# Performance work log

Measured on AMD Instinct MI355X. Metric: run time of the kernel, lower is better.

The kernel has to match this reference:

```python
import jax, jax.numpy as jnp
import numpy as np

D_MODEL = 128
N_HEADS = 8
HEAD_DIM = D_MODEL // N_HEADS
N_EXPERTS = 256
B, T = 4, 512


def rmsnorm(x, gamma, eps=1e-6):
    norm = jnp.sqrt(jnp.mean(jnp.square(x), axis=-1, keepdims=True) + eps)
    return gamma * (x / norm)


def apply_rope(x):
    # x: (B, T, H, D) -- half-split (NeoX-style) rotation
    Bx, Tx, Hx, Dx = x.shape
    inv_freq = 1.0 / (10000.0 ** (jnp.arange(0, Dx, 2, dtype=jnp.float32) / Dx))
    t = jnp.arange(Tx, dtype=jnp.float32)
    freqs = jnp.outer(t, inv_freq)                      # (T, D/2)
    sin_f = jnp.sin(freqs)[None, :, None, :]            # (1, T, 1, D/2)
    cos_f = jnp.cos(freqs)[None, :, None, :]
    x1, x2 = jnp.split(x, 2, axis=-1)
    return jnp.concatenate([x1 * cos_f - x2 * sin_f, x1 * sin_f + x2 * cos_f], axis=-1)


def swiglu(x, w1, b1, w2, b2):
    gate = x @ w1 + b1
    return gate * jax.nn.sigmoid(gate) * (x @ w2 + b2)


def lightning_attention(x, wq, bq, wk, bk, wv, bv, wo, bo):
    Bx, Tx, _ = x.shape
    q = (x @ wq + bq).reshape(Bx, Tx, N_HEADS, HEAD_DIM)
    k = (x @ wk + bk).reshape(Bx, Tx, N_HEADS, HEAD_DIM)
    v = (x @ wv + bv).reshape(Bx, Tx, N_HEADS, HEAD_DIM)
    q = jax.nn.elu(apply_rope(q)) + 1.0
    k = jax.nn.elu(apply_rope(k)) + 1.0
    q = q.transpose(0, 2, 1, 3)  # (B,H,T,D)
    k = k.transpose(0, 2, 1, 3)
    v = v.transpose(0, 2, 1, 3)
    ctx = jnp.einsum('bhtd,bhte->bhde', k, v)           # (B,H,D,D)
    out = jnp.einsum('bhtd,bhde->bhte', q, ctx)         # (B,H,T,D)
    k_sum = jnp.sum(k, axis=2)                          # (B,H,D)
    z = 1.0 / (jnp.einsum('bhtd,bhd->bht', q, k_sum) + 1e-6)
    out = out * z[..., None]
    out = out.transpose(0, 2, 1, 3).reshape(Bx, Tx, D_MODEL)
    return out @ wo + bo


def turbo_quant(x, rot, scale):
    y = x @ rot
    mag = jnp.sqrt(jnp.mean(jnp.square(y), axis=-1, keepdims=True) + 1e-6)
    phase = y / mag
    quant = jnp.round(phase * 8.0) / 8.0
    phase = jax.lax.stop_gradient(quant - phase) + phase  # STE
    return phase * mag * scale


def gated_moe(h, gate_w, gate_b, exp_w, mw1, mb1, mw2, mb2):
    gate_scores = jax.nn.softmax(h @ gate_w + gate_b, axis=-1)       # (B,T,E)
    top_vals, top_idx = jax.lax.top_k(gate_scores, 2)                # (B,T,2)
    top_w = top_vals / (jnp.sum(top_vals, axis=-1, keepdims=True) + 1e-6)
    onehot = jax.nn.one_hot(top_idx, N_EXPERTS, dtype=h.dtype)       # (B,T,2,E)
    mask = jnp.sum(onehot * top_w[..., None], axis=2)                # (B,T,E)
    expert_outputs = jnp.einsum('btd,edo->bteo', h, exp_w)           # (B,T,E,D)
    weighted_avg = jnp.einsum('bteo,bte->bto', expert_outputs, mask)
    weighted_avg = swiglu(weighted_avg, mw1, mb1, mw2, mb2)
    diff_sq = jnp.square(expert_outputs - weighted_avg[:, :, None, :])
    weighted_var = jnp.einsum('bteo,bte->bto', diff_sq, mask)
    consensus = jnp.exp(-jnp.mean(weighted_var, axis=-1))            # (B,T)
    return weighted_avg, consensus


def setup_inputs() -> dict:
    key = jax.random.key(0)
    ks = jax.random.split(key, 24)
    d = D_MODEL
    dw = lambda k, shp: (jax.random.normal(k, shp, dtype=jnp.float32) * 0.02)
    rng = np.random.RandomState(42)
    Q, _ = np.linalg.qr(rng.randn(d, d))
    return {
        'x': jax.random.normal(ks[0], (B, T, d), dtype=jnp.float32),
        'g1': jnp.ones((d,), jnp.float32),
        'wq': dw(ks[1], (d, d)), 'bq': jnp.zeros((d,), jnp.float32),
        'wk': dw(ks[2], (d, d)), 'bk': jnp.zeros((d,), jnp.float32),
        'wv': dw(ks[3], (d, d)), 'bv': jnp.zeros((d,), jnp.float32),
        'wo': dw(ks[4], (d, d)), 'bo': jnp.zeros((d,), jnp.float32),
        'rot': jnp.asarray(Q.astype('float32')),
        'tq_scale': jnp.ones((d,), jnp.float32),
        'sw_w1': dw(ks[5], (d, d)), 'sw_b1': jnp.zeros((d,), jnp.float32),
        'sw_w2': dw(ks[6], (d, d)), 'sw_b2': jnp.zeros((d,), jnp.float32),
        'g2': jnp.ones((d,), jnp.float32),
        'gate_w': dw(ks[7], (d, N_EXPERTS)), 'gate_b': jnp.zeros((N_EXPERTS,), jnp.float32),
        'exp_w': dw(ks[8], (N_EXPERTS, d, d)),
        'moe_w1': dw(ks[9], (d, d)), 'moe_b1': jnp.zeros((d,), jnp.float32),
        'moe_w2': dw(ks[10], (d, d)), 'moe_b2': jnp.zeros((d,), jnp.float32),
    }


def reference(x, g1, wq, bq, wk, bk, wv, bv, wo, bo, rot, tq_scale,
              sw_w1, sw_b1, sw_w2, sw_b2, g2, gate_w, gate_b, exp_w,
              moe_w1, moe_b1, moe_w2, moe_b2):
    attn_out = lightning_attention(rmsnorm(x, g1), wq, bq, wk, bk, wv, bv, wo, bo)
    attn_out = turbo_quant(attn_out, rot, tq_scale)
    x = x + swiglu(attn_out, sw_w1, sw_b1, sw_w2, sw_b2)
    moe_out, consensus = gated_moe(rmsnorm(x, g2), gate_w, gate_b, exp_w,
                                   moe_w1, moe_b1, moe_w2, moe_b2)
    x = x + moe_out
    return x, consensus
```

## Files before the change

kernel.cpp:

```cpp
#include <hip/hip_runtime.h>
#include <math.h>

#define DM 128
#define SEQ 512
#define NTOK 2048
#define NH 8
#define HD 16
#define NE 256
#define CAP 4096

__device__ __forceinline__ float sigmoid_f(float v) { return 1.0f / (1.0f + expf(-v)); }

__device__ __forceinline__ float wave_sum64(float v) {
#pragma unroll
  for (int m = 32; m; m >>= 1) v += __shfl_xor(v, m, 64);
  return v;
}

__global__ __launch_bounds__(512) void k_qkv(
    const float* __restrict__ x, const float* __restrict__ g1,
    const float* __restrict__ wq, const float* __restrict__ bq,
    const float* __restrict__ wk, const float* __restrict__ bk,
    const float* __restrict__ wv, const float* __restrict__ bv_,
    float* __restrict__ q, float* __restrict__ k, float* __restrict__ v) {
  const int tid = threadIdx.x;
  const int o = tid & 127, ks = tid >> 7;
  const int n0 = blockIdx.x * 4;
  __shared__ float h1[4][DM];
  __shared__ float qr[4][DM], kr[4][DM];
  __shared__ float red3[4][4][DM][3];
  __shared__ float wredA[8];

  float xv = x[(n0 + ks) * DM + o];
  float s = wave_sum64(xv * xv);
  if ((tid & 63) == 0) wredA[tid >> 6] = s;
  __syncthreads();
  float tot = wredA[2 * ks] + wredA[2 * ks + 1];
  float rinv = 1.0f / sqrtf(tot * (1.0f / 128.0f) + 1e-6f);
  h1[ks][o] = g1[o] * xv * rinv;
  __syncthreads();

  float aq[4] = {0, 0, 0, 0}, ak[4] = {0, 0, 0, 0}, av[4] = {0, 0, 0, 0};
  const int d0 = ks * 32;
  for (int dd = 0; dd < 32; ++dd) {
    int d = d0 + dd;
    float wqv = wq[d * DM + o], wkv = wk[d * DM + o], wvv = wv[d * DM + o];
#pragma unroll
    for (int g = 0; g < 4; ++g) {
      float hv = h1[g][d];
      aq[g] = fmaf(hv, wqv, aq[g]);
      ak[g] = fmaf(hv, wkv, ak[g]);
      av[g] = fmaf(hv, wvv, av[g]);
    }
  }
#pragma unroll
  for (int g = 0; g < 4; ++g) {
    red3[ks][g][o][0] = aq[g];
    red3[ks][g][o][1] = ak[g];
    red3[ks][g][o][2] = av[g];
  }
  __syncthreads();
  float sq = bq[o], sk = bk[o], sv = bv_[o];
#pragma unroll
  for (int s2 = 0; s2 < 4; ++s2) {
    sq += red3[s2][ks][o][0];
    sk += red3[s2][ks][o][1];
    sv += red3[s2][ks][o][2];
  }
  qr[ks][o] = sq;
  kr[ks][o] = sk;
  v[(n0 + ks) * DM + o] = sv;
  __syncthreads();

  const int i = o & 15, j = i & 7, hi = i & 8, lo = o & ~8;
  const float invf = expf(-(float)j * 1.1512925464970229f);
  int t = (n0 + ks) & (SEQ - 1);
  float ang = (float)t * invf;
  float sn = sinf(ang), cs = cosf(ang);
  float x1q = qr[ks][lo], x2q = qr[ks][lo + 8];
  float x1k = kr[ks][lo], x2k = kr[ks][lo + 8];
  float rq = hi ? (x1q * sn + x2q * cs) : (x1q * cs - x2q * sn);
  float rk = hi ? (x1k * sn + x2k * cs) : (x1k * cs - x2k * sn);
  rq = (rq > 0.0f) ? rq + 1.0f : expf(rq);
  rk = (rk > 0.0f) ? rk + 1.0f : expf(rk);
  q[(n0 + ks) * DM + o] = rq;
  k[(n0 + ks) * DM + o] = rk;
}

__global__ __launch_bounds__(256) void k_ctxp(
    const float* __restrict__ k, const float* __restrict__ v,
    float* __restrict__ ctxp, float* __restrict__ ksump) {
  const int bh = blockIdx.x & 31, tc = blockIdx.x >> 5;
  const int b = bh >> 3, h = bh & 7;
  const int p = threadIdx.x, d = p >> 4, e = p & 15;
  const float* kb = k + (size_t)b * SEQ * DM + h * HD;
  const float* vb = v + (size_t)b * SEQ * DM + h * HD;
  float acc = 0.0f, kss = 0.0f;
  for (int tt = 0; tt < 64; ++tt) {
    int t = tc * 64 + tt;
    float kv = kb[t * DM + d];
    float vv = vb[t * DM + e];
    acc = fmaf(kv, vv, acc);
    kss += kv;
  }
  ctxp[tc * 8192 + bh * 256 + p] = acc;
  if (e == 0) ksump[tc * 512 + bh * HD + d] = kss;
}

__global__ __launch_bounds__(512) void k_attn(
    const float* __restrict__ x, const float* __restrict__ qp,
    const float* __restrict__ ctxp, const float* __restrict__ ksump,
    const float* __restrict__ wo, const float* __restrict__ bo,
    const float* __restrict__ rot, const float* __restrict__ tqs,
    const float* __restrict__ w1, const float* __restrict__ b1,
    const float* __restrict__ w2, const float* __restrict__ b2,
    const float* __restrict__ g2,
    float* __restrict__ xmid, float* __restrict__ h2o) {
  const int tid = threadIdx.x;
  const int o = tid & 127, ks = tid >> 7;
  const int n0 = blockIdx.x * 4;
  const int b = n0 >> 9;
  __shared__ float ctxs[NH * 256];
  __shared__ float kss[DM];
  __shared__ float rowA[4][DM], rowB[4][DM];
  __shared__ float red2[4][4][DM][2];
  __shared__ float wredA[8], wredB[8];

  for (int idx = tid; idx < 2048; idx += 512) {
    float s = 0.0f;
#pragma unroll
    for (int tc = 0; tc < 8; ++tc) s += ctxp[tc * 8192 + b * 2048 + idx];
    ctxs[idx] = s;
  }
  if (tid < 128) {
    float s = 0.0f;
#pragma unroll
    for (int tc = 0; tc < 8; ++tc) s += ksump[tc * 512 + b * DM + tid];
    kss[tid] = s;
  }
  rowA[ks][o] = qp[(n0 + ks) * DM + o];
  __syncthreads();

  {
    int h = o >> 4, e = o & 15;
    float oa = 0.0f, qk = 0.0f;
#pragma unroll
    for (int d = 0; d < HD; ++d) {
      float qv = rowA[ks][h * HD + d];
      oa = fmaf(qv, ctxs[h * 256 + d * 16 + e], oa);
      qk = fmaf(qv, kss[h * HD + d], qk);
    }
    rowB[ks][o] = oa / (qk + 1e-6f);
  }
  __syncthreads();

  const int d0 = ks * 32;
  {
    float acc[4] = {0, 0, 0, 0};
    for (int dd = 0; dd < 32; ++dd) {
      int d = d0 + dd;
      float w = wo[d * DM + o];
#pragma unroll
      for (int g = 0; g < 4; ++g) acc[g] = fmaf(rowB[g][d], w, acc[g]);
    }
#pragma unroll
    for (int g = 0; g < 4; ++g) red2[ks][g][o][0] = acc[g];
  }
  __syncthreads();
  {
    float sa = bo[o];
#pragma unroll
    for (int s2 = 0; s2 < 4; ++s2) sa += red2[s2][ks][o][0];
    rowA[ks][o] = sa;
  }
  __syncthreads();

  {
    float acc[4] = {0, 0, 0, 0};
    for (int dd = 0; dd < 32; ++dd) {
      int d = d0 + dd;
      float r = rot[d * DM + o];
#pragma unroll
      for (int g = 0; g < 4; ++g) acc[g] = fmaf(rowA[g][d], r, acc[g]);
    }
#pragma unroll
    for (int g = 0; g < 4; ++g) red2[ks][g][o][1] = acc[g];
  }
  __syncthreads();
  {
    float y = 0.0f;
#pragma unroll
    for (int s2 = 0; s2 < 4; ++s2) y += red2[s2][ks][o][1];
    float ssq = wave_sum64(y * y);
    if ((tid & 63) == 0) wredA[tid >> 6] = ssq;
    __syncthreads();
    float tot = wredA[2 * ks] + wredA[2 * ks + 1];
    float mag = sqrtf(tot * (1.0f / 128.0f) + 1e-6f);
    float phase = y / mag;
    rowB[ks][o] = rintf(phase * 8.0f) * 0.125f * mag * tqs[o];
  }
  __syncthreads();

  {
    float a1[4] = {0, 0, 0, 0}, a2[4] = {0, 0, 0, 0};
    for (int dd = 0; dd < 32; ++dd) {
      int d = d0 + dd;
      float w1v = w1[d * DM + o];
      float w2v = w2[d * DM + o];
#pragma unroll
      for (int g = 0; g < 4; ++g) {
        float t = rowB[g][d];
        a1[g] = fmaf(t, w1v, a1[g]);
        a2[g] = fmaf(t, w2v, a2[g]);
      }
    }
#pragma unroll
    for (int g = 0; g < 4; ++g) {
      red2[ks][g][o][0] = a1[g];
      red2[ks][g][o][1] = a2[g];
    }
  }
  __syncthreads();
  {
    float ga = b1[o], up = b2[o];
#pragma unroll
    for (int s2 = 0; s2 < 4; ++s2) {
      ga += red2[s2][ks][o][0];
      up += red2[s2][ks][o][1];
    }
    float swv = ga * sigmoid_f(ga) * up;
    float xm = x[(n0 + ks) * DM + o] + swv;
    xmid[(n0 + ks) * DM + o] = xm;
    float ssq = wave_sum64(xm * xm);
    if ((tid & 63) == 0) wredB[tid >> 6] = ssq;
    __syncthreads();
    float tot = wredB[2 * ks] + wredB[2 * ks + 1];
    float rinv = 1.0f / sqrtf(tot * (1.0f / 128.0f) + 1e-6f);
    h2o[(n0 + ks) * DM + o] = g2[o] * xm * rinv;
  }
}

__global__ __launch_bounds__(1024) void k_gate(
    const float* __restrict__ h2, const float* __restrict__ gate_w,
    const float* __restrict__ gate_b,
    float* __restrict__ tw, int* __restrict__ cnt, int* __restrict__ list) {
  const int tid = threadIdx.x;
  const int n0 = blockIdx.x * 4;
  __shared__ float h2s[4][DM];
  __shared__ float redg[4][4][NE];
  __shared__ float lgl[4][NE];

  if (tid < 512) {
    int g = tid >> 7, o = tid & 127;
    h2s[g][o] = h2[(n0 + g) * DM + o];
  }
  __syncthreads();

  {
    int e = tid & 255, kq = tid >> 8;
    float lg[4] = {0, 0, 0, 0};
    for (int dd = 0; dd < 32; ++dd) {
      int d = kq * 32 + dd;
      float gw = gate_w[d * NE + e];
#pragma unroll
      for (int g = 0; g < 4; ++g) lg[g] = fmaf(h2s[g][d], gw, lg[g]);
    }
#pragma unroll
    for (int g = 0; g < 4; ++g) redg[kq][g][e] = lg[g];
  }
  __syncthreads();
  {
    int e = tid & 255, kq = tid >> 8;
    float lf = gate_b[e];
#pragma unroll
    for (int s2 = 0; s2 < 4; ++s2) lf += redg[s2][kq][e];
    lgl[kq][e] = lf;
  }
  __syncthreads();

  if (tid < 256) {
    int lane = tid & 63, g = tid >> 6;
    float bv = -INFINITY;
    int bi = 0;
#pragma unroll
    for (int j2 = 0; j2 < 4; ++j2) {
      int e = lane + 64 * j2;
      float vv = lgl[g][e];
      if (vv > bv || (vv == bv && e < bi)) { bv = vv; bi = e; }
    }
#pragma unroll
    for (int m = 32; m; m >>= 1) {
      float pv = __shfl_xor(bv, m, 64);
      int pi = __shfl_xor(bi, m, 64);
      if (pv > bv || (pv == bv && pi < bi)) { bv = pv; bi = pi; }
    }
    float se = 0.0f;
#pragma unroll
    for (int j2 = 0; j2 < 4; ++j2) se += expf(lgl[g][lane + 64 * j2] - bv);
    se = wave_sum64(se);
    float mv = -INFINITY;
    int mi = 0;
#pragma unroll
    for (int j2 = 0; j2 < 4; ++j2) {
      int e = lane + 64 * j2;
      if (e != bi) {
        float vv = lgl[g][e];
        if (vv > mv || (vv == mv && e < mi)) { mv = vv; mi = e; }
      }
    }
#pragma unroll
    for (int m = 32; m; m >>= 1) {
      float pv = __shfl_xor(mv, m, 64);
      int pi = __shfl_xor(mi, m, 64);
      if (pv > mv || (pv == mv && pi < mi)) { mv = pv; mi = pi; }
    }
    if (lane == 0) {
      float v0 = 1.0f / se;
      float v1 = expf(mv - bv) / se;
      float wsum = v0 + v1 + 1e-6f;
      int t = n0 + g;
      tw[t * 2 + 0] = v0 / wsum;
      tw[t * 2 + 1] = v1 / wsum;
      int r0 = atomicAdd(&cnt[bi], 1);
      list[bi * CAP + r0] = t * 2 + 0;
      int r1 = atomicAdd(&cnt[mi], 1);
      list[mi * CAP + r1] = t * 2 + 1;
    }
  }
}

__global__ __launch_bounds__(512) void k_exp(
    const float* __restrict__ h2, const float* __restrict__ exp_w,
    const int* __restrict__ cnt, const int* __restrict__ list,
    float* __restrict__ elbuf) {
  const int e = blockIdx.x;
  const int nt = cnt[e];
  if (nt == 0) return;
  const int tid = threadIdx.x;
  const int o = tid & 127, qq = tid >> 7;
  const float* W = exp_w + (size_t)e * (DM * DM);
  float wreg[32];
#pragma unroll
  for (int dd = 0; dd < 32; ++dd) wreg[dd] = W[(qq * 32 + dd) * DM + o];
  __shared__ float h2t[8][DM];
  __shared__ float psum[4][8][DM];
  __shared__ int alst[8];

  for (int i0 = 0; i0 < nt; i0 += 8) {
    int gn = min(8, nt - i0);
    for (int idx = tid; idx < gn * 128; idx += 512) {
      int j = idx >> 7;
      int a = list[e * CAP + i0 + j];
      h2t[j][idx & 127] = h2[(size_t)(a >> 1) * DM + (idx & 127)];
    }
    if (tid < gn) alst[tid] = list[e * CAP + i0 + tid];
    __syncthreads();
    for (int j = 0; j < gn; ++j) {
      const float4* hp = (const float4*)&h2t[j][qq * 32];
      float acc = 0.0f;
#pragma unroll
      for (int d4 = 0; d4 < 8; ++d4) {
        float4 hv = hp[d4];
        acc = fmaf(wreg[d4 * 4 + 0], hv.x, acc);
        acc = fmaf(wreg[d4 * 4 + 1], hv.y, acc);
        acc = fmaf(wreg[d4 * 4 + 2], hv.z, acc);
        acc = fmaf(wreg[d4 * 4 + 3], hv.w, acc);
      }
      psum[qq][j][o] = acc;
    }
    __syncthreads();
    for (int j = qq; j < gn; j += 4) {
      float r = psum[0][j][o] + psum[1][j][o] + psum[2][j][o] + psum[3][j][o];
      elbuf[(size_t)alst[j] * DM + o] = r;
    }
    __syncthreads();
  }
}

__global__ __launch_bounds__(512) void k_comb(
    const float* __restrict__ elbuf, const float* __restrict__ tw,
    const float* __restrict__ xmid,
    const float* __restrict__ mw1, const float* __restrict__ mb1,
    const float* __restrict__ mw2, const float* __restrict__ mb2,
    float* __restrict__ out_x, float* __restrict__ out_cons) {
  const int tid = threadIdx.x;
  const int g = tid >> 7, o = tid & 127;
  const int t = blockIdx.x * 4 + g;
  __shared__ float was[4][DM];
  __shared__ float wredV[8];
  float w0 = tw[t * 2 + 0], w1 = tw[t * 2 + 1];
  float el0 = elbuf[(size_t)(t * 2 + 0) * DM + o];
  float el1 = elbuf[(size_t)(t * 2 + 1) * DM + o];
  was[g][o] = w0 * el0 + w1 * el1;
  __syncthreads();
  float a1 = mb1[o], a2 = mb2[o];
  for (int d = 0; d < DM; ++d) {
    float tt = was[g][d];
    a1 = fmaf(tt, mw1[d * DM + o], a1);
    a2 = fmaf(tt, mw2[d * DM + o], a2);
  }
  float swv = a1 * sigmoid_f(a1) * a2;
  out_x[(size_t)t * DM + o] = xmid[(size_t)t * DM + o] + swv;
  float dd0 = el0 - swv, dd1 = el1 - swv;
  float vt = wave_sum64(w0 * dd0 * dd0 + w1 * dd1 * dd1);
  if ((tid & 63) == 0) wredV[tid >> 6] = vt;
  __syncthreads();
  if (tid < 4)
    out_cons[blockIdx.x * 4 + tid] =
        expf(-(wredV[2 * tid] + wredV[2 * tid + 1]) * (1.0f / 128.0f));
}

extern "C" void kernel_launch(void* const* d_in, const int* in_sizes, int n_in,
                              void* d_out, int out_size, void* d_ws, size_t ws_size,
                              hipStream_t stream) {
  const float* x = (const float*)d_in[0];
  const float* g1 = (const float*)d_in[1];
  const float* wq = (const float*)d_in[2];
  const float* bq = (const float*)d_in[3];
  const float* wk = (const float*)d_in[4];
  const float* bk = (const float*)d_in[5];
  const float* wv = (const float*)d_in[6];
  const float* bv = (const float*)d_in[7];
  const float* wo = (const float*)d_in[8];
  const float* bo = (const float*)d_in[9];
  const float* rot = (const float*)d_in[10];
  const float* tqs = (const float*)d_in[11];
  const float* sw1 = (const float*)d_in[12];
  const float* sb1 = (const float*)d_in[13];
  const float* sw2 = (const float*)d_in[14];
  const float* sb2 = (const float*)d_in[15];
  const float* g2 = (const float*)d_in[16];
  const float* gw = (const float*)d_in[17];
  const float* gb = (const float*)d_in[18];
  const float* ew = (const float*)d_in[19];
  const float* mw1 = (const float*)d_in[20];
  const float* mb1 = (const float*)d_in[21];
  const float* mw2 = (const float*)d_in[22];
  const float* mb2 = (const float*)d_in[23];

  float* ws = (float*)d_ws;
  float* q = ws;
  float* k = ws + 262144;
  float* v = ws + 524288;
  float* ctxp = ws + 786432;
  float* ksump = ws + 851968;
  float* xmid = ws + 856064;
  float* h2 = ws + 1118208;
  float* tw = ws + 1380352;
  float* elbuf = ws + 1384448;
  int* cnt = (int*)(ws + 1908736);
  int* list = (int*)(ws + 1908992);
  float* out_x = (float*)d_out;
  float* out_c = out_x + (size_t)NTOK * DM;

  hipMemsetAsync(cnt, 0, NE * sizeof(int), stream);
  hipLaunchKernelGGL(k_qkv, dim3(NTOK / 4), dim3(512), 0, stream,
                     x, g1, wq, bq, wk, bk, wv, bv, q, k, v);
  hipLaunchKernelGGL(k_ctxp, dim3(256), dim3(256), 0, stream, k, v, ctxp, ksump);
  hipLaunchKernelGGL(k_attn, dim3(NTOK / 4), dim3(512), 0, stream,
                     x, q, ctxp, ksump, wo, bo, rot, tqs, sw1, sb1, sw2, sb2, g2,
                     xmid, h2);
  hipLaunchKernelGGL(k_gate, dim3(NTOK / 4), dim3(1024), 0, stream,
                     h2, gw, gb, tw, cnt, list);
  hipLaunchKernelGGL(k_exp, dim3(NE), dim3(512), 0, stream,
                     h2, ew, cnt, list, elbuf);
  hipLaunchKernelGGL(k_comb, dim3(NTOK / 4), dim3(512), 0, stream,
                     elbuf, tw, xmid, mw1, mb1, mw2, mb2, out_x, out_c);
}
```

Measured before the change: 75.34 us.

## Fuse gating into attention kernel, drop memset, split-K the combine kernel

Moves the MoE gate logits, top-2 selection and expert list building into the tail of the attention kernel, reusing the h2 rows already in shared memory. This removes one kernel launch and the global reload of h2. The cnt buffer is now zeroed inside the first kernel instead of by a separate memset. The combine kernel grows to 1024 threads with a two-way split-K over the SwiGLU matmul. In exchange, the attention kernel uses more shared memory and does more work per block, which may lower occupancy.

Result: faster. 68.57 us (-9.0%).

```diff
diff --git a/kernel.cpp b/kernel.cpp
--- a/kernel.cpp
+++ b/kernel.cpp
@@ -22,7 +22,8 @@
     const float* __restrict__ wq, const float* __restrict__ bq,
     const float* __restrict__ wk, const float* __restrict__ bk,
     const float* __restrict__ wv, const float* __restrict__ bv_,
-    float* __restrict__ q, float* __restrict__ k, float* __restrict__ v) {
+    float* __restrict__ q, float* __restrict__ k, float* __restrict__ v,
+    int* __restrict__ cnt) {
   const int tid = threadIdx.x;
   const int o = tid & 127, ks = tid >> 7;
   const int n0 = blockIdx.x * 4;
@@ -30,6 +31,8 @@
   __shared__ float qr[4][DM], kr[4][DM];
   __shared__ float red3[4][4][DM][3];
   __shared__ float wredA[8];
+
+  if (blockIdx.x == 0 && tid < NE) cnt[tid] = 0;
 
   float xv = x[(n0 + ks) * DM + o];
   float s = wave_sum64(xv * xv);
@@ -115,7 +118,9 @@
     const float* __restrict__ w1, const float* __restrict__ b1,
     const float* __restrict__ w2, const float* __restrict__ b2,
     const float* __restrict__ g2,
-    float* __restrict__ xmid, float* __restrict__ h2o) {
+    const float* __restrict__ gate_w, const float* __restrict__ gate_b,
+    float* __restrict__ xmid, float* __restrict__ h2o,
+    float* __restrict__ tw, int* __restrict__ cnt, int* __restrict__ list) {
   const int tid = threadIdx.x;
   const int o = tid & 127, ks = tid >> 7;
   const int n0 = blockIdx.x * 4;
@@ -124,6 +129,8 @@
   __shared__ float kss[DM];
   __shared__ float rowA[4][DM], rowB[4][DM];
   __shared__ float red2[4][4][DM][2];
+  __shared__ float redg[2][4][NE];
+  __shared__ float lgl[4][NE];
   __shared__ float wredA[8], wredB[8];
 
   for (int idx = tid; idx < 2048; idx += 512) {
@@ -236,45 +243,33 @@
     __syncthreads();
     float tot = wredB[2 * ks] + wredB[2 * ks + 1];
     float rinv = 1.0f / sqrtf(tot * (1.0f / 128.0f) + 1e-6f);
-    h2o[(n0 + ks) * DM + o] = g2[o] * xm * rinv;
-  }
-}
-
-__global__ __launch_bounds__(1024) void k_gate(
-    const float* __restrict__ h2, const float* __restrict__ gate_w,
-    const float* __restrict__ gate_b,
-    float* __restrict__ tw, int* __restrict__ cnt, int* __restrict__ list) {
-  const int tid = threadIdx.x;
-  const int n0 = blockIdx.x * 4;
-  __shared__ float h2s[4][DM];
-  __shared__ float redg[4][4][NE];
-  __shared__ float lgl[4][NE];
-
-  if (tid < 512) {
-    int g = tid >> 7, o = tid & 127;
-    h2s[g][o] = h2[(n0 + g) * DM + o];
+    float h2v = g2[o] * xm * rinv;
+    h2o[(n0 + ks) * DM + o] = h2v;
+    rowA[ks][o] = h2v;
   }
   __syncthreads();
 
   {
     int e = tid & 255, kq = tid >> 8;
     float lg[4] = {0, 0, 0, 0};
-    for (int dd = 0; dd < 32; ++dd) {
-      int d = kq * 32 + dd;
-      float gw = gate_w[d * NE + e];
-#pragma unroll
-      for (int g = 0; g < 4; ++g) lg[g] = fmaf(h2s[g][d], gw, lg[g]);
+    for (int dd = 0; dd < 64; ++dd) {
+      int d = kq * 64 + dd;
+      float gwv = gate_w[d * NE + e];
+#pragma unroll
+      for (int g = 0; g < 4; ++g) lg[g] = fmaf(rowA[g][d], gwv, lg[g]);
     }
 #pragma unroll
     for (int g = 0; g < 4; ++g) redg[kq][g][e] = lg[g];
   }
   __syncthreads();
   {
-    int e = tid & 255, kq = tid >> 8;
-    float lf = gate_b[e];
-#pragma unroll
-    for (int s2 = 0; s2 < 4; ++s2) lf += redg[s2][kq][e];
-    lgl[kq][e] = lf;
+    int e = tid & 255, half = tid >> 8;
+    float gbv = gate_b[e];
+#pragma unroll
+    for (int gg2 = 0; gg2 < 2; ++gg2) {
+      int g = half * 2 + gg2;
+      lgl[g][e] = redg[0][g][e] + redg[1][g][e] + gbv;
+    }
   }
   __syncthreads();
 
@@ -377,36 +372,58 @@
   }
 }
 
-__global__ __launch_bounds__(512) void k_comb(
+__global__ __launch_bounds__(1024) void k_comb(
     const float* __restrict__ elbuf, const float* __restrict__ tw,
     const float* __restrict__ xmid,
     const float* __restrict__ mw1, const float* __restrict__ mb1,
     const float* __restrict__ mw2, const float* __restrict__ mb2,
     float* __restrict__ out_x, float* __restrict__ out_cons) {
   const int tid = threadIdx.x;
-  const int g = tid >> 7, o = tid & 127;
-  const int t = blockIdx.x * 4 + g;
+  const int n0 = blockIdx.x * 4;
   __shared__ float was[4][DM];
+  __shared__ float els[4][2][DM];
+  __shared__ float redm[2][4][DM][2];
   __shared__ float wredV[8];
-  float w0 = tw[t * 2 + 0], w1 = tw[t * 2 + 1];
-  float el0 = elbuf[(size_t)(t * 2 + 0) * DM + o];
-  float el1 = elbuf[(size_t)(t * 2 + 1) * DM + o];
-  was[g][o] = w0 * el0 + w1 * el1;
-  __syncthreads();
-  float a1 = mb1[o], a2 = mb2[o];
-  for (int d = 0; d < DM; ++d) {
-    float tt = was[g][d];
-    a1 = fmaf(tt, mw1[d * DM + o], a1);
-    a2 = fmaf(tt, mw2[d * DM + o], a2);
-  }
-  float swv = a1 * sigmoid_f(a1) * a2;
-  out_x[(size_t)t * DM + o] = xmid[(size_t)t * DM + o] + swv;
-  float dd0 = el0 - swv, dd1 = el1 - swv;
-  float vt = wave_sum64(w0 * dd0 * dd0 + w1 * dd1 * dd1);
-  if ((tid & 63) == 0) wredV[tid >> 6] = vt;
+
+  if (tid < 512) {
+    int g = tid >> 7, o = tid & 127;
+    int t = n0 + g;
+    float w0 = tw[t * 2 + 0], w1 = tw[t * 2 + 1];
+    float el0 = elbuf[(size_t)(t * 2 + 0) * DM + o];
+    float el1 = elbuf[(size_t)(t * 2 + 1) * DM + o];
+    els[g][0][o] = el0;
+    els[g][1][o] = el1;
+    was[g][o] = w0 * el0 + w1 * el1;
+  }
+  __syncthreads();
+  {
+    int kh = tid >> 9, r = tid & 511, g = r >> 7, o = r & 127;
+    float a1 = 0.0f, a2 = 0.0f;
+    for (int dd = 0; dd < 64; ++dd) {
+      int d = kh * 64 + dd;
+      float t = was[g][d];
+      a1 = fmaf(t, mw1[d * DM + o], a1);
+      a2 = fmaf(t, mw2[d * DM + o], a2);
+    }
+    redm[kh][g][o][0] = a1;
+    redm[kh][g][o][1] = a2;
+  }
+  __syncthreads();
+  if (tid < 512) {
+    int g = tid >> 7, o = tid & 127;
+    int t = n0 + g;
+    float ga = redm[0][g][o][0] + redm[1][g][o][0] + mb1[o];
+    float up = redm[0][g][o][1] + redm[1][g][o][1] + mb2[o];
+    float swv = ga * sigmoid_f(ga) * up;
+    out_x[(size_t)t * DM + o] = xmid[(size_t)t * DM + o] + swv;
+    float w0 = tw[t * 2 + 0], w1 = tw[t * 2 + 1];
+    float dd0 = els[g][0][o] - swv, dd1 = els[g][1][o] - swv;
+    float vt = wave_sum64(w0 * dd0 * dd0 + w1 * dd1 * dd1);
+    if ((tid & 63) == 0) wredV[tid >> 6] = vt;
+  }
   __syncthreads();
   if (tid < 4)
-    out_cons[blockIdx.x * 4 + tid] =
+    out_cons[n0 + tid] =
         expf(-(wredV[2 * tid] + wredV[2 * tid + 1]) * (1.0f / 128.0f));
 }
 
@@ -453,17 +470,14 @@
   float* out_x = (float*)d_out;
   float* out_c = out_x + (size_t)NTOK * DM;
 
-  hipMemsetAsync(cnt, 0, NE * sizeof(int), stream);
   hipLaunchKernelGGL(k_qkv, dim3(NTOK / 4), dim3(512), 0, stream,
-                     x, g1, wq, bq, wk, bk, wv, bv, q, k, v);
+                     x, g1, wq, bq, wk, bk, wv, bv, q, k, v, cnt);
   hipLaunchKernelGGL(k_ctxp, dim3(256), dim3(256), 0, stream, k, v, ctxp, ksump);
   hipLaunchKernelGGL(k_attn, dim3(NTOK / 4), dim3(512), 0, stream,
                      x, q, ctxp, ksump, wo, bo, rot, tqs, sw1, sb1, sw2, sb2, g2,
-                     xmid, h2);
-  hipLaunchKernelGGL(k_gate, dim3(NTOK / 4), dim3(1024), 0, stream,
-                     h2, gw, gb, tw, cnt, list);
+                     gw, gb, xmid, h2, tw, cnt, list);
   hipLaunchKernelGGL(k_exp, dim3(NE), dim3(512), 0, stream,
                      h2, ew, cnt, list, elbuf);
-  hipLaunchKernelGGL(k_comb, dim3(NTOK / 4), dim3(512), 0, stream,
+  hipLaunchKernelGGL(k_comb, dim3(NTOK / 4), dim3(1024), 0, stream,
                      elbuf, tw, xmid, mw1, mb1, mw2, mb2, out_x, out_c);
 }
```
